# Performance work log

Hardware: AMD Instinct MI355X
Metric: run time of the kernel (lower is better)

## Reference

```python
import jax, jax.numpy as jnp
import numpy as np

D_MODEL = 1024
D_INNER = 2048   # expand * d_model
D_STATE = 16
DT_RANK = 64     # ceil(d_model / 16)
D_CONV = 4
L = 2048
EPS = 1e-5


def setup_inputs() -> dict:
    key = jax.random.key(0)
    ks = jax.random.split(key, 8)
    sc = lambda k, shape: jax.random.normal(k, shape, jnp.float32) * 0.02
    A = jnp.tile(jnp.arange(1, D_STATE + 1, dtype=jnp.float32), (D_INNER, 1))
    return {
        "x": jax.random.normal(ks[0], (L, D_MODEL), jnp.float32),
        "W_in": sc(ks[1], (D_MODEL, 2 * D_INNER)),          # in_proj (no bias)
        "W_conv": sc(ks[2], (D_CONV, D_INNER)),             # depthwise conv kernel
        "b_conv": jnp.zeros((D_INNER,), jnp.float32),
        "W_x": sc(ks[3], (D_INNER, DT_RANK + 2 * D_STATE)), # x_proj (no bias)
        "W_dt": sc(ks[4], (DT_RANK, D_INNER)),
        "b_dt": jnp.zeros((D_INNER,), jnp.float32),
        "A_log": jnp.log(A),
        "D": jnp.ones((D_INNER,), jnp.float32),
        "W_out": sc(ks[5], (D_INNER, D_MODEL)),             # out_proj (no bias)
        "ln_scale": jnp.ones((D_MODEL,), jnp.float32),
        "ln_bias": jnp.zeros((D_MODEL,), jnp.float32),
        "drop_key": 0,  # unused: training=False -> DropPath is identity
    }


def reference(x, W_in, W_conv, b_conv, W_x, W_dt, b_dt, A_log, D, W_out,
              ln_scale, ln_bias, drop_key):
    l = x.shape[0]
    # LayerNorm (flax default: mean/var over features)
    mu = jnp.mean(x, axis=-1, keepdims=True)
    var = jnp.mean(jnp.square(x), axis=-1, keepdims=True) - jnp.square(mu)
    xn = (x - mu) * jax.lax.rsqrt(var + EPS) * ln_scale + ln_bias

    # MambaBlock
    xr = xn @ W_in                         # (l, 2*d_inner)
    u, res = xr[:, :D_INNER], xr[:, D_INNER:]

    # causal depthwise conv: pad left d_conv-1, take first l outputs
    up = jnp.pad(u, ((D_CONV - 1, 0), (0, 0)))
    uc = b_conv + sum(up[k:k + l] * W_conv[k] for k in range(D_CONV))
    u2 = jax.nn.silu(uc)                   # (l, d_inner)

    # SSM params (input-dependent)
    x_dbl = u2 @ W_x                       # (l, dt_rank + 2n)
    dt = x_dbl[:, :DT_RANK]
    B = x_dbl[:, DT_RANK:DT_RANK + D_STATE]
    C = x_dbl[:, DT_RANK + D_STATE:]
    delta = jax.nn.softplus(dt @ W_dt + b_dt)   # (l, d_inner)
    A = -jnp.exp(A_log)                         # (d_inner, n)

    dA = jnp.exp(jnp.einsum('ld,dn->ldn', delta, A))   # (l, d_inner, n)
    dBu = jnp.einsum('ld,ln->ldn', delta * u2, B)       # (l, d_inner, n)

    def step(h, inp):
        dA_t, dBu_t, C_t = inp
        h = dA_t * h + dBu_t               # (d_inner, n)
        return h, h @ C_t                  # y_t: (d_inner,)

    h0 = jnp.zeros((D_INNER, D_STATE), dtype=u2.dtype)
    _, ys = jax.lax.scan(step, h0, (dA, dBu, C))
    y = ys + u2 * D                        # (l, d_inner)

    y = y * jax.nn.silu(res)
    out = y @ W_out                        # (l, d_model)
    return out + x                         # residual (DropPath identity in eval)
```

## Files before the change

kernel.cpp:

```cpp
#include <hip/hip_runtime.h>
#include <math.h>

#define L_SEQ 2048
#define DM 1024
#define DI 2048
#define DS 16
#define DTR 64
#define EPS 1e-5f
#define NSEG 32
#define SEGLEN 64
#define NSTATE (DI * DS)

typedef float f32x4 __attribute__((ext_vector_type(4)));
typedef __bf16 bf16x8 __attribute__((ext_vector_type(8)));
typedef _Float16 h16x2 __attribute__((ext_vector_type(2)));

static __device__ __forceinline__ unsigned short f2bf(float f) {
  union { float f; unsigned u; } v; v.f = f;
  unsigned r = v.u + 0x7fffu + ((v.u >> 16) & 1u);
  return (unsigned short)(r >> 16);
}
static __device__ __forceinline__ float bf2f(unsigned short s) {
  union { unsigned u; float f; } v; v.u = ((unsigned)s) << 16;
  return v.f;
}

static __device__ __forceinline__ void gload16(const void* g, void* l) {
  __builtin_amdgcn_global_load_lds(
      (__attribute__((address_space(1))) void*)(unsigned long long)(g),
      (__attribute__((address_space(3))) void*)(unsigned)(unsigned long long)(l),
      16, 0, 0);
}

__global__ __launch_bounds__(256) void ln_kernel(const float* __restrict__ x,
                                                 const float* __restrict__ sc,
                                                 const float* __restrict__ bi,
                                                 unsigned short* __restrict__ xnb) {
  int row = blockIdx.x;
  int t = threadIdx.x;
  float4 xv = ((const float4*)(x + (size_t)row * DM))[t];
  float s  = xv.x + xv.y + xv.z + xv.w;
  float s2 = xv.x*xv.x + xv.y*xv.y + xv.z*xv.z + xv.w*xv.w;
  #pragma unroll
  for (int m = 32; m >= 1; m >>= 1) {
    s  += __shfl_xor(s, m);
    s2 += __shfl_xor(s2, m);
  }
  __shared__ float red[8];
  int wid = t >> 6, lane = t & 63;
  if (lane == 0) { red[wid] = s; red[4 + wid] = s2; }
  __syncthreads();
  s  = red[0] + red[1] + red[2] + red[3];
  s2 = red[4] + red[5] + red[6] + red[7];
  float mu = s * (1.f / DM);
  float var = s2 * (1.f / DM) - mu * mu;
  float rs = rsqrtf(var + EPS);
  float4 sc4 = ((const float4*)sc)[t];
  float4 bi4 = ((const float4*)bi)[t];
  ushort4 ob;
  ob.x = f2bf((xv.x - mu) * rs * sc4.x + bi4.x);
  ob.y = f2bf((xv.y - mu) * rs * sc4.y + bi4.y);
  ob.z = f2bf((xv.z - mu) * rs * sc4.z + bi4.z);
  ob.w = f2bf((xv.w - mu) * rs * sc4.w + bi4.w);
  *(ushort4*)&xnb[(size_t)row * DM + t * 4] = ob;
}

__global__ __launch_bounds__(256) void trans_bf16(
    const float* __restrict__ W, unsigned short* __restrict__ Wt, int K, int N)
{
  __shared__ unsigned short s[64][80];
  int n0 = blockIdx.x * 64, k0 = blockIdx.y * 64;
  int tid = threadIdx.x;
  #pragma unroll
  for (int p = 0; p < 4; ++p) {
    int i = p * 16 + (tid >> 4);
    int j = (tid & 15) * 4;
    float4 w = *(const float4*)&W[(size_t)(k0 + i) * N + n0 + j];
    s[j + 0][i] = f2bf(w.x); s[j + 1][i] = f2bf(w.y);
    s[j + 2][i] = f2bf(w.z); s[j + 3][i] = f2bf(w.w);
  }
  __syncthreads();
  #pragma unroll
  for (int q = 0; q < 2; ++q) {
    int n = q * 32 + (tid >> 3);
    int i8 = (tid & 7) * 8;
    *(int4*)&Wt[(size_t)(n0 + n) * K + k0 + i8] = *(const int4*)&s[n][i8];
  }
}

__global__ __launch_bounds__(256) void transpose_b16(
    const unsigned short* __restrict__ in, unsigned short* __restrict__ out,
    int R, int C)
{
  __shared__ unsigned short s[64][72];
  int c0 = blockIdx.x * 64, r0 = blockIdx.y * 64;
  int tid = threadIdx.x;
  #pragma unroll
  for (int p = 0; p < 2; ++p) {
    int r = p * 32 + (tid >> 3);
    int c = (tid & 7) * 8;
    *(int4*)&s[r][c] = *(const int4*)&in[(size_t)(r0 + r) * C + c0 + c];
  }
  __syncthreads();
  #pragma unroll
  for (int p = 0; p < 2; ++p) {
    int c = p * 32 + (tid >> 3);
    int r = (tid & 7) * 8;
    ushort4 a, b;
    a.x = s[r + 0][c]; a.y = s[r + 1][c]; a.z = s[r + 2][c]; a.w = s[r + 3][c];
    b.x = s[r + 4][c]; b.y = s[r + 5][c]; b.z = s[r + 6][c]; b.w = s[r + 7][c];
    *(ushort4*)&out[(size_t)(c0 + c) * R + r0 + r] = a;
    *(ushort4*)&out[(size_t)(c0 + c) * R + r0 + r + 4] = b;
  }
}

__global__ __launch_bounds__(256) void trans_wx(
    const float* __restrict__ Wx, unsigned short* __restrict__ Wxt)
{
  int i = blockIdx.x * 256 + threadIdx.x;
  int n = i >> 11, k = i & 2047;
  Wxt[i] = (n < 96) ? f2bf(Wx[(size_t)k * 96 + n]) : (unsigned short)0;
}

template<int BM, int BN, int EPI, int OUTB, int SPLITK>
__global__ __launch_bounds__(256) void gemm2(
    const unsigned short* __restrict__ A, int lda,
    const unsigned short* __restrict__ Bt, int ldb,
    void* __restrict__ Cv, int ldc,
    int M, int N, int K,
    const float* __restrict__ bias)
{
  constexpr int WM = BM / 2, WN = BN / 2;
  constexpr int FM = WM / 16, FN = WN / 16;
  __shared__ __align__(16) unsigned short smA[BM * 64];
  __shared__ __align__(16) unsigned short smB[BN * 64];

  int nwg = gridDim.x * gridDim.y;
  int bid = blockIdx.y * gridDim.x + blockIdx.x;
  if ((nwg & 7) == 0) {
    int cpx = nwg >> 3;
    bid = (bid & 7) * cpx + (bid >> 3);
  }
  int bx = bid % gridDim.x;
  int by = bid / gridDim.x;
  int m0 = by * BM, n0 = bx * BN;

  int tid = threadIdx.x;
  int lane = tid & 63, wid = tid >> 6;
  int wm = wid >> 1, wn = wid & 1;

  int kb = blockIdx.z * (K / SPLITK);
  int nt = (K / SPLITK) / 64;

  int rs = lane >> 3;
  int cs = (lane & 7) * 8;

  f32x4 acc[FM][FN];
  #pragma unroll
  for (int m = 0; m < FM; ++m)
    #pragma unroll
    for (int n = 0; n < FN; ++n) acc[m][n] = (f32x4){0.f, 0.f, 0.f, 0.f};

  for (int kt = 0; kt < nt; ++kt) {
    __syncthreads();
    #pragma unroll
    for (int i = 0; i < BM / 32; ++i) {
      int chunk = wid * (BM / 32) + i;
      gload16(A + (size_t)(m0 + chunk * 8 + rs) * lda + kb + kt * 64 + cs,
              (char*)smA + chunk * 1024);
    }
    #pragma unroll
    for (int i = 0; i < BN / 32; ++i) {
      int chunk = wid * (BN / 32) + i;
      gload16(Bt + (size_t)(n0 + chunk * 8 + rs) * ldb + kb + kt * 64 + cs,
              (char*)smB + chunk * 1024);
    }
    __syncthreads();

    #pragma unroll
    for (int kk = 0; kk < 2; ++kk) {
      bf16x8 aF[FM], bF[FN];
      #pragma unroll
      for (int m = 0; m < FM; ++m) {
        int r = wm * WM + m * 16 + (lane & 15);
        aF[m] = *(const bf16x8*)((const char*)smA + r * 128 + kk * 64 + (lane >> 4) * 16);
      }
      #pragma unroll
      for (int n = 0; n < FN; ++n) {
        int r = wn * WN + n * 16 + (lane & 15);
        bF[n] = *(const bf16x8*)((const char*)smB + r * 128 + kk * 64 + (lane >> 4) * 16);
      }
      #pragma unroll
      for (int m = 0; m < FM; ++m)
        #pragma unroll
        for (int n = 0; n < FN; ++n)
          acc[m][n] = __builtin_amdgcn_mfma_f32_16x16x32_bf16(
              aF[m], bF[n], acc[m][n], 0, 0, 0);
    }
  }

  float* Cf = (float*)Cv + (size_t)blockIdx.z * M * ldc;
  unsigned short* Cb = (unsigned short*)Cv;
  int cm = (lane >> 4) * 4, cn = lane & 15;
  #pragma unroll
  for (int m = 0; m < FM; ++m)
    #pragma unroll
    for (int n = 0; n < FN; ++n) {
      int col = n0 + wn * WN + n * 16 + cn;
      #pragma unroll
      for (int r = 0; r < 4; ++r) {
        int row = m0 + wm * WM + m * 16 + cm + r;
        float v = acc[m][n][r];
        if (EPI == 1) {
          float w = v + bias[row];
          v = (w > 20.f) ? w : log1pf(__expf(w));
        }
        if (OUTB) Cb[(size_t)row * ldc + col] = f2bf(v);
        else      Cf[(size_t)row * ldc + col] = v;
      }
    }
}

__global__ __launch_bounds__(256) void xdbl_reduce(
    const float* __restrict__ part, unsigned short* __restrict__ xdbl)
{
  int i = (blockIdx.x * 256 + threadIdx.x) * 4;
  const int SL = 2048 * 128;
  float4 s = *(const float4*)&part[i];
  #pragma unroll
  for (int z = 1; z < 16; ++z) {
    float4 p = *(const float4*)&part[(size_t)z * SL + i];
    s.x += p.x; s.y += p.y; s.z += p.z; s.w += p.w;
  }
  ushort4 ob;
  ob.x = f2bf(s.x); ob.y = f2bf(s.y); ob.z = f2bf(s.z); ob.w = f2bf(s.w);
  *(ushort4*)&xdbl[i] = ob;
}

__global__ __launch_bounds__(256) void out_reduce(
    const float* __restrict__ part, const float* __restrict__ x,
    float* __restrict__ out)
{
  int i = (blockIdx.x * 256 + threadIdx.x) * 4;
  const int SL = 2048 * 1024;
  float4 a = *(const float4*)&part[i];
  float4 b = *(const float4*)&part[SL + i];
  float4 r = *(const float4*)&x[i];
  float4 o;
  o.x = a.x + b.x + r.x; o.y = a.y + b.y + r.y;
  o.z = a.z + b.z + r.z; o.w = a.w + b.w + r.w;
  *(float4*)&out[i] = o;
}

__global__ __launch_bounds__(256) void conv_silu_fused(
    const unsigned short* __restrict__ xrT,
    const float* __restrict__ Wc, const float* __restrict__ bc,
    unsigned short* __restrict__ u2T, unsigned short* __restrict__ u2b)
{
  __shared__ unsigned short st[128][68];
  int d0 = blockIdx.x * 64, l0 = blockIdx.y * 128;
  int tid = threadIdx.x;
  int dloc = tid & 63;
  int lp = (tid >> 6) * 32;
  int d = d0 + dloc;
  const unsigned short* ur = xrT + (size_t)d * L_SEQ + l0 + lp;
  float w0 = Wc[0 * DI + d], w1 = Wc[1 * DI + d];
  float w2 = Wc[2 * DI + d], w3 = Wc[3 * DI + d];
  float b = bc[d];

  ushort4 vin[8];
  #pragma unroll
  for (int j = 0; j < 8; ++j) vin[j] = *(const ushort4*)&ur[j * 4];
  ushort4 vh; vh.x = vh.y = vh.z = vh.w = 0;
  if (l0 + lp > 0) vh = *(const ushort4*)&ur[-4];
  float prev3 = bf2f(vh.y), prev2 = bf2f(vh.z), prev1 = bf2f(vh.w);

  #pragma unroll
  for (int j = 0; j < 8; ++j) {
    float xs[4] = {bf2f(vin[j].x), bf2f(vin[j].y), bf2f(vin[j].z), bf2f(vin[j].w)};
    ushort4 ob;
    unsigned short* o = (unsigned short*)&ob;
    #pragma unroll
    for (int i = 0; i < 4; ++i) {
      float y = b + w0 * prev3 + w1 * prev2 + w2 * prev1 + w3 * xs[i];
      prev3 = prev2; prev2 = prev1; prev1 = xs[i];
      float sig = 1.f / (1.f + __expf(-y));
      o[i] = f2bf(y * sig);
    }
    *(ushort4*)&u2T[(size_t)d * L_SEQ + l0 + lp + j * 4] = ob;
    st[lp + j * 4 + 0][dloc] = o[0];
    st[lp + j * 4 + 1][dloc] = o[1];
    st[lp + j * 4 + 2][dloc] = o[2];
    st[lp + j * 4 + 3][dloc] = o[3];
  }
  __syncthreads();
  int lr = tid >> 1, hf = (tid & 1) * 32;
  unsigned short* ob = &u2b[(size_t)(l0 + lr) * DI + d0 + hf];
  *(int4*)&ob[0]  = *(const int4*)&st[lr][hf + 0];
  *(int4*)&ob[8]  = *(const int4*)&st[lr][hf + 8];
  *(int4*)&ob[16] = *(const int4*)&st[lr][hf + 16];
  *(int4*)&ob[24] = *(const int4*)&st[lr][hf + 24];
}


__global__ __launch_bounds__(128) void scan_pass1(
    const unsigned short* __restrict__ deltaT, const unsigned short* __restrict__ u2T,
    const unsigned short* __restrict__ xdbl,
    const float* __restrict__ A_log,
    float* __restrict__ hend, float* __restrict__ aprod)
{
  int t = threadIdx.x;
  int ch = t >> 4, n = t & 15;
  int li = (t & 15) * 4;
  int d0 = blockIdx.x * 8, d = d0 + ch;
  int base = blockIdx.y * SEGLEN;

  __shared__ __align__(16) float sdT[8][68], suT[8][68], sBT[16][68];

  float An = -__expf(A_log[d * DS + n]);

  ushort4 rdu = *(const ushort4*)&deltaT[(size_t)d * L_SEQ + base + li];
  ushort4 ru  = *(const ushort4*)&u2T[(size_t)d * L_SEQ + base + li];
  ushort4 rB[2];
  #pragma unroll
  for (int q = 0; q < 2; ++q) {
    int ll = base + (t >> 2) + q * 32;
    rB[q] = *(const ushort4*)&xdbl[(size_t)ll * 128 + 64 + (t & 3) * 4];
  }

  float d0v = bf2f(rdu.x), d1v = bf2f(rdu.y), d2v = bf2f(rdu.z), d3v = bf2f(rdu.w);
  sdT[ch][li + 0] = d0v; sdT[ch][li + 1] = d1v;
  sdT[ch][li + 2] = d2v; sdT[ch][li + 3] = d3v;
  suT[ch][li + 0] = d0v * bf2f(ru.x); suT[ch][li + 1] = d1v * bf2f(ru.y);
  suT[ch][li + 2] = d2v * bf2f(ru.z); suT[ch][li + 3] = d3v * bf2f(ru.w);
  #pragma unroll
  for (int q = 0; q < 2; ++q) {
    int ll = (t >> 2) + q * 32;
    int nb = (t & 3) * 4;
    sBT[nb + 0][ll] = bf2f(rB[q].x); sBT[nb + 1][ll] = bf2f(rB[q].y);
    sBT[nb + 2][ll] = bf2f(rB[q].z); sBT[nb + 3][ll] = bf2f(rB[q].w);
  }
  __syncthreads();

  float h = 0.f, sdl = 0.f;
  #pragma unroll
  for (int g = 0; g < 64; g += 4) {
    float4 dl4 = *(const float4*)&sdT[ch][g];
    float4 du4 = *(const float4*)&suT[ch][g];
    float4 Bn4 = *(const float4*)&sBT[n][g];
    float dl[4] = {dl4.x, dl4.y, dl4.z, dl4.w};
    float du[4] = {du4.x, du4.y, du4.z, du4.w};
    float Bn[4] = {Bn4.x, Bn4.y, Bn4.z, Bn4.w};
    #pragma unroll
    for (int i = 0; i < 4; ++i) {
      float dA = __expf(dl[i] * An);
      sdl += dl[i];
      h = dA * h + du[i] * Bn[i];
    }
  }
  size_t idx = (size_t)blockIdx.y * NSTATE + d0 * DS + t;
  hend[idx]  = h;
  aprod[idx] = __expf(An * sdl);
}

__global__ __launch_bounds__(256) void scan_pass2(
    const float* __restrict__ hend, const float* __restrict__ aprod,
    float* __restrict__ h_in)
{
  int i = blockIdx.x * 256 + threadIdx.x;
  float h = 0.f;
  h_in[i] = 0.f;
  for (int s = 0; s < NSEG - 1; ++s) {
    h = aprod[(size_t)s * NSTATE + i] * h + hend[(size_t)s * NSTATE + i];
    h_in[(size_t)(s + 1) * NSTATE + i] = h;
  }
}

__global__ __launch_bounds__(128) void scan_pass3(
    const unsigned short* __restrict__ deltaT, const unsigned short* __restrict__ u2T,
    const unsigned short* __restrict__ resT,
    const unsigned short* __restrict__ xdbl,
    const float* __restrict__ A_log, const float* __restrict__ Dp,
    const float* __restrict__ h_in,
    unsigned short* __restrict__ ybT)
{
  int t = threadIdx.x;
  int ch = t >> 4, n = t & 15;
  int li = (t & 15) * 4;
  int d0 = blockIdx.x * 8, d = d0 + ch;
  int s = blockIdx.y;
  int base = s * SEGLEN;

  __shared__ __align__(16) float sdT[8][68], suT[8][68];
  __shared__ __align__(16) float sBT[16][68], sCT[16][68];
  __shared__ __align__(4) _Float16 svh[32][134];

  float An = -__expf(A_log[d * DS + n]);
  float h = h_in[(size_t)s * NSTATE + d0 * DS + t];

  ushort4 rdu = *(const ushort4*)&deltaT[(size_t)d * L_SEQ + base + li];
  ushort4 ru  = *(const ushort4*)&u2T[(size_t)d * L_SEQ + base + li];
  ushort4 rB[2], rC[2];
  #pragma unroll
  for (int q = 0; q < 2; ++q) {
    int ll = base + (t >> 2) + q * 32;
    int n4 = (t & 3) * 4;
    rB[q] = *(const ushort4*)&xdbl[(size_t)ll * 128 + 64 + n4];
    rC[q] = *(const ushort4*)&xdbl[(size_t)ll * 128 + 80 + n4];
  }

  float d0v = bf2f(rdu.x), d1v = bf2f(rdu.y), d2v = bf2f(rdu.z), d3v = bf2f(rdu.w);
  sdT[ch][li + 0] = d0v; sdT[ch][li + 1] = d1v;
  sdT[ch][li + 2] = d2v; sdT[ch][li + 3] = d3v;
  suT[ch][li + 0] = d0v * bf2f(ru.x); suT[ch][li + 1] = d1v * bf2f(ru.y);
  suT[ch][li + 2] = d2v * bf2f(ru.z); suT[ch][li + 3] = d3v * bf2f(ru.w);
  #pragma unroll
  for (int q = 0; q < 2; ++q) {
    int ll = (t >> 2) + q * 32;
    int nb = (t & 3) * 4;
    sBT[nb + 0][ll] = bf2f(rB[q].x); sBT[nb + 1][ll] = bf2f(rB[q].y);
    sBT[nb + 2][ll] = bf2f(rB[q].z); sBT[nb + 3][ll] = bf2f(rB[q].w);
    sCT[nb + 0][ll] = bf2f(rC[q].x); sCT[nb + 1][ll] = bf2f(rC[q].y);
    sCT[nb + 2][ll] = bf2f(rC[q].z); sCT[nb + 3][ll] = bf2f(rC[q].w);
  }
  __syncthreads();

  #pragma unroll
  for (int half = 0; half < 2; ++half) {
    int g0 = half * 32;
    #pragma unroll
    for (int g = g0; g < g0 + 32; g += 4) {
      float4 dl4 = *(const float4*)&sdT[ch][g];
      float4 du4 = *(const float4*)&suT[ch][g];
      float4 Bn4 = *(const float4*)&sBT[n][g];
      float4 Cn4 = *(const float4*)&sCT[n][g];
      float dl[4] = {dl4.x, dl4.y, dl4.z, dl4.w};
      float du[4] = {du4.x, du4.y, du4.z, du4.w};
      float Bn[4] = {Bn4.x, Bn4.y, Bn4.z, Bn4.w};
      float Cn[4] = {Cn4.x, Cn4.y, Cn4.z, Cn4.w};
      #pragma unroll
      for (int i = 0; i < 4; ++i) {
        float dA = __expf(dl[i] * An);
        h = dA * h + du[i] * Bn[i];
        svh[g - g0 + i][t] = (_Float16)(h * Cn[i]);
      }
    }
    __syncthreads();

    #pragma unroll
    for (int r = 0; r < 2; ++r) {
      int idx = r * 128 + t;
      int ll = idx & 31, c2 = idx >> 5;
      const _Float16* row = &svh[ll][c2 * 16];
      float sum = 0.f;
      #pragma unroll
      for (int k = 0; k < 8; ++k) {
        h16x2 pv = *(const h16x2*)&row[k * 2];
        sum += (float)pv.x + (float)pv.y;
      }
      int dd = d0 + c2;
      int lg = base + g0 + ll;
      float uv = bf2f(u2T[(size_t)dd * L_SEQ + lg]);
      float rv = bf2f(resT[(size_t)dd * L_SEQ + lg]);
      float sig = 1.f / (1.f + __expf(-rv));
      float yv = (sum + uv * Dp[dd]) * rv * sig;
      ybT[(size_t)dd * L_SEQ + lg] = f2bf(yv);
    }
    __syncthreads();
  }
}

extern "C" void kernel_launch(void* const* d_in, const int* in_sizes, int n_in,
                              void* d_out, int out_size, void* d_ws, size_t ws_size,
                              hipStream_t stream)
{
  const float* x      = (const float*)d_in[0];
  const float* W_in   = (const float*)d_in[1];
  const float* W_conv = (const float*)d_in[2];
  const float* b_conv = (const float*)d_in[3];
  const float* W_x    = (const float*)d_in[4];
  const float* W_dt   = (const float*)d_in[5];
  const float* b_dt   = (const float*)d_in[6];
  const float* A_log  = (const float*)d_in[7];
  const float* Dp     = (const float*)d_in[8];
  const float* W_out  = (const float*)d_in[9];
  const float* ln_s   = (const float*)d_in[10];
  const float* ln_b   = (const float*)d_in[11];

  char* ws = (char*)d_ws;
  const size_t MB = 1u << 20;
  unsigned short* xnb    = (unsigned short*)(ws);
  unsigned short* xrT    = (unsigned short*)(ws + 4 * MB);
  unsigned short* u2T    = (unsigned short*)(ws + 20 * MB);
  unsigned short* u2b    = (unsigned short*)(ws + 28 * MB);
  float*          hend   = (float*)(ws + 28 * MB);
  float*          aprod  = (float*)(ws + 32 * MB);
  unsigned short* xdbl   = (unsigned short*)(ws + 36 * MB);
  unsigned short* Wxt    = (unsigned short*)(ws + 36 * MB + 512 * 1024);
  unsigned short* Wdt_t  = (unsigned short*)(ws + 37 * MB);
  unsigned short* deltaTb= (unsigned short*)(ws + 38 * MB);
  unsigned short* Wtin   = (unsigned short*)(ws + 38 * MB);
  float*          part   = (float*)(ws + 46 * MB);
  unsigned short* ybT    = (unsigned short*)(ws + 54 * MB);
  float*          h_in   = (float*)(ws + 62 * MB);
  unsigned short* yb     = (unsigned short*)(ws + 4 * MB);
  unsigned short* Wtout  = xnb;
  const unsigned short* resT = xrT + (size_t)DI * L_SEQ;

  ln_kernel<<<L_SEQ, 256, 0, stream>>>(x, ln_s, ln_b, xnb);

  trans_bf16<<<dim3((2 * DI) / 64, DM / 64), 256, 0, stream>>>(W_in, Wtin, DM, 2 * DI);

  gemm2<128, 128, 0, 1, 1><<<dim3(L_SEQ / 128, (2 * DI) / 128), 256, 0, stream>>>(
      Wtin, DM, xnb, DM, xrT, L_SEQ, 2 * DI, L_SEQ, DM, nullptr);

  conv_silu_fused<<<dim3(DI / 64, L_SEQ / 128), 256, 0, stream>>>(
      xrT, W_conv, b_conv, u2T, u2b);

  trans_wx<<<(128 * 2048) / 256, 256, 0, stream>>>(W_x, Wxt);

  gemm2<64, 128, 0, 0, 16><<<dim3(1, L_SEQ / 64, 16), 256, 0, stream>>>(
      u2b, DI, Wxt, DI, part, 128, L_SEQ, 128, DI, nullptr);

  xdbl_reduce<<<(L_SEQ * 128) / 1024, 256, 0, stream>>>(part, xdbl);

  trans_bf16<<<dim3(DI / 64, DTR / 64), 256, 0, stream>>>(W_dt, Wdt_t, DTR, DI);

  gemm2<64, 128, 1, 1, 1><<<dim3(L_SEQ / 128, DI / 64), 256, 0, stream>>>(
      Wdt_t, DTR, xdbl, 128, deltaTb, L_SEQ, DI, L_SEQ, DTR, b_dt);

  trans_bf16<<<dim3(DM / 64, DI / 64), 256, 0, stream>>>(W_out, Wtout, DI, DM);

  scan_pass1<<<dim3(DI / 8, NSEG - 1), 128, 0, stream>>>(
      deltaTb, u2T, xdbl, A_log, hend, aprod);

  scan_pass2<<<NSTATE / 256, 256, 0, stream>>>(hend, aprod, h_in);

  scan_pass3<<<dim3(DI / 8, NSEG), 128, 0, stream>>>(
      deltaTb, u2T, resT, xdbl, A_log, Dp, h_in, ybT);

  transpose_b16<<<dim3(L_SEQ / 64, DI / 64), 256, 0, stream>>>(ybT, yb, DI, L_SEQ);

  gemm2<64, 128, 0, 0, 2><<<dim3(DM / 128, L_SEQ / 64, 2), 256, 0, stream>>>(
      yb, DI, Wtout, DI, part, DM, L_SEQ, DM, DI, nullptr);

  out_reduce<<<(L_SEQ * DM) / 1024, 256, 0, stream>>>(part, x, (float*)d_out);
}
```

Baseline: 183.8 us.

## Merge weight prep kernels, stage bf16 GEMM output via LDS, fuse y transpose

Replaces the four separate weight-conversion launches with one prep_weights kernel that dispatches tiles by block index, moving W_out to its own workspace region so it can be prepared up front. The bf16-output GEMM epilogue now stages results in shared memory and writes 16-byte coalesced rows instead of scattered 2-byte stores. scan_pass3 writes y directly in row-major layout through a small shared tile, removing the standalone transpose kernel. This reduces launch count and uncoalesced traffic, at the cost of extra syncs and narrow 16-byte row writes per timestep in the scan.

```diff
diff --git a/kernel.cpp b/kernel.cpp
--- a/kernel.cpp
+++ b/kernel.cpp
@@ -65,11 +65,11 @@
   *(ushort4*)&xnb[(size_t)row * DM + t * 4] = ob;
 }
 
-__global__ __launch_bounds__(256) void trans_bf16(
-    const float* __restrict__ W, unsigned short* __restrict__ Wt, int K, int N)
+static __device__ __forceinline__ void trans_tile(
+    const float* __restrict__ W, unsigned short* __restrict__ Wt,
+    int K, int N, int n0, int k0)
 {
   __shared__ unsigned short s[64][80];
-  int n0 = blockIdx.x * 64, k0 = blockIdx.y * 64;
   int tid = threadIdx.x;
   #pragma unroll
   for (int p = 0; p < 4; ++p) {
@@ -88,38 +88,31 @@
   }
 }
 
-__global__ __launch_bounds__(256) void transpose_b16(
-    const unsigned short* __restrict__ in, unsigned short* __restrict__ out,
-    int R, int C)
-{
-  __shared__ unsigned short s[64][72];
-  int c0 = blockIdx.x * 64, r0 = blockIdx.y * 64;
-  int tid = threadIdx.x;
-  #pragma unroll
-  for (int p = 0; p < 2; ++p) {
-    int r = p * 32 + (tid >> 3);
-    int c = (tid & 7) * 8;
-    *(int4*)&s[r][c] = *(const int4*)&in[(size_t)(r0 + r) * C + c0 + c];
-  }
-  __syncthreads();
-  #pragma unroll
-  for (int p = 0; p < 2; ++p) {
-    int c = p * 32 + (tid >> 3);
-    int r = (tid & 7) * 8;
-    ushort4 a, b;
-    a.x = s[r + 0][c]; a.y = s[r + 1][c]; a.z = s[r + 2][c]; a.w = s[r + 3][c];
-    b.x = s[r + 4][c]; b.y = s[r + 5][c]; b.z = s[r + 6][c]; b.w = s[r + 7][c];
-    *(ushort4*)&out[(size_t)(c0 + c) * R + r0 + r] = a;
-    *(ushort4*)&out[(size_t)(c0 + c) * R + r0 + r + 4] = b;
-  }
-}
-
-__global__ __launch_bounds__(256) void trans_wx(
-    const float* __restrict__ Wx, unsigned short* __restrict__ Wxt)
-{
-  int i = blockIdx.x * 256 + threadIdx.x;
-  int n = i >> 11, k = i & 2047;
-  Wxt[i] = (n < 96) ? f2bf(Wx[(size_t)k * 96 + n]) : (unsigned short)0;
+__global__ __launch_bounds__(256) void prep_weights(
+    const float* __restrict__ W_in, const float* __restrict__ W_out,
+    const float* __restrict__ W_dt, const float* __restrict__ Wx,
+    unsigned short* __restrict__ Wtin, unsigned short* __restrict__ Wtout,
+    unsigned short* __restrict__ Wdt_t, unsigned short* __restrict__ Wxt)
+{
+  int b = blockIdx.x;
+  if (b < 1024) {
+    trans_tile(W_in, Wtin, DM, 2 * DI, (b & 63) * 64, (b >> 6) * 64);
+  } else if (b < 1536) {
+    int r = b - 1024;
+    trans_tile(W_out, Wtout, DI, DM, (r & 15) * 64, (r >> 4) * 64);
+  } else if (b < 1568) {
+    int r = b - 1536;
+    trans_tile(W_dt, Wdt_t, DTR, DI, r * 64, 0);
+  } else {
+    int r = b - 1568;
+    int i = r * 256 + threadIdx.x;
+    #pragma unroll
+    for (int p = 0; p < 64; ++p) {
+      int ii = i + p * 4096;
+      int n = ii >> 11, k = ii & 2047;
+      Wxt[ii] = (n < 96) ? f2bf(Wx[(size_t)k * 96 + n]) : (unsigned short)0;
+    }
+  }
 }
 
 template<int BM, int BN, int EPI, int OUTB, int SPLITK>
@@ -132,8 +125,9 @@
 {
   constexpr int WM = BM / 2, WN = BN / 2;
   constexpr int FM = WM / 16, FN = WN / 16;
-  __shared__ __align__(16) unsigned short smA[BM * 64];
-  __shared__ __align__(16) unsigned short smB[BN * 64];
+  __shared__ __align__(16) unsigned short sm[(BM + BN) * 64];
+  unsigned short* smA = sm;
+  unsigned short* smB = sm + BM * 64;
 
   int nwg = gridDim.x * gridDim.y;
   int bid = blockIdx.y * gridDim.x + blockIdx.x;
@@ -199,26 +193,52 @@
     }
   }
 
-  float* Cf = (float*)Cv + (size_t)blockIdx.z * M * ldc;
-  unsigned short* Cb = (unsigned short*)Cv;
   int cm = (lane >> 4) * 4, cn = lane & 15;
-  #pragma unroll
-  for (int m = 0; m < FM; ++m)
-    #pragma unroll
-    for (int n = 0; n < FN; ++n) {
-      int col = n0 + wn * WN + n * 16 + cn;
-      #pragma unroll
-      for (int r = 0; r < 4; ++r) {
-        int row = m0 + wm * WM + m * 16 + cm + r;
-        float v = acc[m][n][r];
-        if (EPI == 1) {
-          float w = v + bias[row];
-          v = (w > 20.f) ? w : log1pf(__expf(w));
+  if (OUTB) {
+    unsigned short* Cb = (unsigned short*)Cv;
+    __syncthreads();
+    #pragma unroll
+    for (int m = 0; m < FM; ++m)
+      #pragma unroll
+      for (int n = 0; n < FN; ++n) {
+        int col = wn * WN + n * 16 + cn;
+        #pragma unroll
+        for (int r = 0; r < 4; ++r) {
+          int row = wm * WM + m * 16 + cm + r;
+          float v = acc[m][n][r];
+          if (EPI == 1) {
+            float w = v + bias[m0 + row];
+            v = (w > 20.f) ? w : log1pf(__expf(w));
+          }
+          sm[row * BN + col] = f2bf(v);
         }
-        if (OUTB) Cb[(size_t)row * ldc + col] = f2bf(v);
-        else      Cf[(size_t)row * ldc + col] = v;
       }
-    }
+    __syncthreads();
+    constexpr int NI4 = BM * BN / 8;
+    for (int k = tid; k < NI4; k += 256) {
+      int row = k / (BN / 8);
+      int c8 = (k % (BN / 8)) * 8;
+      *(int4*)&Cb[(size_t)(m0 + row) * ldc + n0 + c8] = *(const int4*)&sm[row * BN + c8];
+    }
+  } else {
+    float* Cf = (float*)Cv + (size_t)blockIdx.z * M * ldc;
+    #pragma unroll
+    for (int m = 0; m < FM; ++m)
+      #pragma unroll
+      for (int n = 0; n < FN; ++n) {
+        int col = n0 + wn * WN + n * 16 + cn;
+        #pragma unroll
+        for (int r = 0; r < 4; ++r) {
+          int row = m0 + wm * WM + m * 16 + cm + r;
+          float v = acc[m][n][r];
+          if (EPI == 1) {
+            float w = v + bias[row];
+            v = (w > 20.f) ? w : log1pf(__expf(w));
+          }
+          Cf[(size_t)row * ldc + col] = v;
+        }
+      }
+  }
 }
 
 __global__ __launch_bounds__(256) void xdbl_reduce(
@@ -382,7 +402,7 @@
     const unsigned short* __restrict__ xdbl,
     const float* __restrict__ A_log, const float* __restrict__ Dp,
     const float* __restrict__ h_in,
-    unsigned short* __restrict__ ybT)
+    unsigned short* __restrict__ yb)
 {
   int t = threadIdx.x;
   int ch = t >> 4, n = t & 15;
@@ -394,6 +414,7 @@
   __shared__ __align__(16) float sdT[8][68], suT[8][68];
   __shared__ __align__(16) float sBT[16][68], sCT[16][68];
   __shared__ __align__(4) _Float16 svh[32][134];
+  __shared__ __align__(16) unsigned short syt[32][8];
 
   float An = -__expf(A_log[d * DS + n]);
   float h = h_in[(size_t)s * NSTATE + d0 * DS + t];
@@ -463,10 +484,13 @@
       float uv = bf2f(u2T[(size_t)dd * L_SEQ + lg]);
       float rv = bf2f(resT[(size_t)dd * L_SEQ + lg]);
       float sig = 1.f / (1.f + __expf(-rv));
-      float yv = (sum + uv * Dp[dd]) * rv * sig;
-      ybT[(size_t)dd * L_SEQ + lg] = f2bf(yv);
+      syt[ll][c2] = f2bf((sum + uv * Dp[dd]) * rv * sig);
     }
     __syncthreads();
+    if (t < 32) {
+      int lg = base + g0 + t;
+      *(int4*)&yb[(size_t)lg * DI + d0] = *(const int4*)&syt[t][0];
+    }
   }
 }
 
@@ -501,15 +525,15 @@
   unsigned short* deltaTb= (unsigned short*)(ws + 38 * MB);
   unsigned short* Wtin   = (unsigned short*)(ws + 38 * MB);
   float*          part   = (float*)(ws + 46 * MB);
-  unsigned short* ybT    = (unsigned short*)(ws + 54 * MB);
   float*          h_in   = (float*)(ws + 62 * MB);
+  unsigned short* Wtout  = (unsigned short*)(ws + 66 * MB);
   unsigned short* yb     = (unsigned short*)(ws + 4 * MB);
-  unsigned short* Wtout  = xnb;
   const unsigned short* resT = xrT + (size_t)DI * L_SEQ;
 
+  prep_weights<<<1584, 256, 0, stream>>>(W_in, W_out, W_dt, W_x,
+                                          Wtin, Wtout, Wdt_t, Wxt);
+
   ln_kernel<<<L_SEQ, 256, 0, stream>>>(x, ln_s, ln_b, xnb);
-
-  trans_bf16<<<dim3((2 * DI) / 64, DM / 64), 256, 0, stream>>>(W_in, Wtin, DM, 2 * DI);
 
   gemm2<128, 128, 0, 1, 1><<<dim3(L_SEQ / 128, (2 * DI) / 128), 256, 0, stream>>>(
       Wtin, DM, xnb, DM, xrT, L_SEQ, 2 * DI, L_SEQ, DM, nullptr);
@@ -517,29 +541,21 @@
   conv_silu_fused<<<dim3(DI / 64, L_SEQ / 128), 256, 0, stream>>>(
       xrT, W_conv, b_conv, u2T, u2b);
 
-  trans_wx<<<(128 * 2048) / 256, 256, 0, stream>>>(W_x, Wxt);
-
   gemm2<64, 128, 0, 0, 16><<<dim3(1, L_SEQ / 64, 16), 256, 0, stream>>>(
       u2b, DI, Wxt, DI, part, 128, L_SEQ, 128, DI, nullptr);
 
   xdbl_reduce<<<(L_SEQ * 128) / 1024, 256, 0, stream>>>(part, xdbl);
 
-  trans_bf16<<<dim3(DI / 64, DTR / 64), 256, 0, stream>>>(W_dt, Wdt_t, DTR, DI);
-
   gemm2<64, 128, 1, 1, 1><<<dim3(L_SEQ / 128, DI / 64), 256, 0, stream>>>(
       Wdt_t, DTR, xdbl, 128, deltaTb, L_SEQ, DI, L_SEQ, DTR, b_dt);
 
-  trans_bf16<<<dim3(DM / 64, DI / 64), 256, 0, stream>>>(W_out, Wtout, DI, DM);
-
   scan_pass1<<<dim3(DI / 8, NSEG - 1), 128, 0, stream>>>(
       deltaTb, u2T, xdbl, A_log, hend, aprod);
 
   scan_pass2<<<NSTATE / 256, 256, 0, stream>>>(hend, aprod, h_in);
 
   scan_pass3<<<dim3(DI / 8, NSEG), 128, 0, stream>>>(
-      deltaTb, u2T, resT, xdbl, A_log, Dp, h_in, ybT);
-
-  transpose_b16<<<dim3(L_SEQ / 64, DI / 64), 256, 0, stream>>>(ybT, yb, DI, L_SEQ);
+      deltaTb, u2T, resT, xdbl, A_log, Dp, h_in, yb);
 
   gemm2<64, 128, 0, 0, 2><<<dim3(DM / 128, L_SEQ / 64, 2), 256, 0, stream>>>(
       yb, DI, Wtout, DI, part, DM, L_SEQ, DM, DI, nullptr);
```

New measurement: 178.4 us. 2.9% less time.
